# Performance work log

Hardware: AMD Instinct MI355X
Metric: run time of the kernel (lower is better)

Reference implementation:

```python
import jax, jax.numpy as jnp
import numpy as np

NEG_SLOPE = 0.2  # PyG GATConv default negative_slope
EPS = 1e-16     # PyG softmax denominator epsilon


def gat_conv(x, src, dst, W, a_src, a_dst, bias):
    """PyG GATConv (concat=True, dropout off). x:[N,Fin], src/dst:[E]."""
    N = x.shape[0]
    H, C = a_src.shape
    h = (x @ W).reshape(N, H, C)                      # per-head projected features
    es = jnp.einsum('nhc,hc->nh', h, a_src)           # alpha_src per node/head
    ed = jnp.einsum('nhc,hc->nh', h, a_dst)           # alpha_dst per node/head
    e = jax.nn.leaky_relu(es[src] + ed[dst], NEG_SLOPE)   # [E,H] edge scores
    # segment softmax over destination nodes (every node has a self loop)
    m = jax.ops.segment_max(e, dst, num_segments=N)
    p = jnp.exp(e - m[dst])
    denom = jax.ops.segment_sum(p, dst, num_segments=N)
    alpha = p / (denom[dst] + EPS)                    # [E,H]
    out = jax.ops.segment_sum(h[src] * alpha[:, :, None], dst, num_segments=N)
    return out.reshape(N, H * C) + bias


def _single_graph(x, ei, W1, a_src1, a_dst1, b1, W2, a_src2, a_dst2, b2):
    N = x.shape[0]
    loop = jnp.arange(N, dtype=ei.dtype)              # add_self_loops=True
    src = jnp.concatenate([ei[0], loop])
    dst = jnp.concatenate([ei[1], loop])
    h = jax.nn.relu(gat_conv(x, src, dst, W1, a_src1, a_dst1, b1))
    # F.dropout with p=0.0 is identity
    return gat_conv(h, src, dst, W2, a_src2, a_dst2, b2)


def setup_inputs() -> dict:
    key = jax.random.key(0)
    ks = jax.random.split(key, 9)
    B, N, E, F_in, H, C = 2, 20000, 320000, 128, 8, 64

    def glorot(k, shape):
        fan_in, fan_out = shape[-2] if len(shape) > 1 else shape[-1], shape[-1]
        s = np.sqrt(6.0 / (fan_in + fan_out)).astype(np.float32)
        return jax.random.uniform(k, shape, jnp.float32, -s, s)

    return {
        'xs': jax.random.normal(ks[0], (B, N, F_in), jnp.float32),
        'edge_indexs': jax.random.randint(ks[1], (B, 2, E), 0, N, jnp.int32),
        'W1': glorot(ks[2], (F_in, H * C)),
        'a_src1': glorot(ks[3], (H, C)),
        'a_dst1': glorot(ks[4], (H, C)),
        'b1': jnp.zeros((H * C,), jnp.float32),
        'W2': glorot(ks[5], (H * C, C)),
        'a_src2': glorot(ks[6], (1, C)),
        'a_dst2': glorot(ks[7], (1, C)),
        'b2': jnp.zeros((C,), jnp.float32),
    }


def reference(xs, edge_indexs, W1, a_src1, a_dst1, b1, W2, a_src2, a_dst2, b2):
    f = lambda x, ei: _single_graph(x, ei, W1, a_src1, a_dst1, b1, W2, a_src2, a_dst2, b2)
    return jax.vmap(f)(xs, edge_indexs)               # [B, N, C]
```

## Files before the change

kernel.cpp:

```cpp
#include <hip/hip_runtime.h>
#include <hip/hip_bf16.h>
#include <cstdint>

#define NEG_SLOPE 0.2f
#define SOFTMAX_EPS 1e-16f
#define NN 20000
#define EE 320000
#define CAP 48

typedef __hip_bfloat16 bf16;
typedef unsigned short ushort;
typedef short s8v __attribute__((ext_vector_type(8)));
typedef float f4v __attribute__((ext_vector_type(4)));
typedef float f2v __attribute__((ext_vector_type(2)));

static __device__ __forceinline__ float lo16(unsigned u) { return __uint_as_float(u << 16); }
static __device__ __forceinline__ float hi16(unsigned u) { return __uint_as_float(u & 0xffff0000u); }
static __device__ __forceinline__ ushort f2bf(float v) {
    bf16 h = __float2bfloat16(v);
    return *(ushort*)&h;
}

__global__ void prep_kernel(const float* __restrict__ W1, const float* __restrict__ W2,
                            ushort* __restrict__ w1hi, ushort* __restrict__ w1lo,
                            ushort* __restrict__ w2hi, ushort* __restrict__ w2lo,
                            int* __restrict__ count) {
    int bid = blockIdx.x;
    int t = threadIdx.x;
    if (bid >= 48) {
        int idx = (bid - 48) * 256 + t;
        if (idx < 2 * NN) count[idx] = 0;
        return;
    }
    __shared__ float T[32][65];
    const float* src; ushort *dhi, *dlo; int K, C, c0, k0;
    if (bid < 32) { src = W1; dhi = w1hi; dlo = w1lo; K = 128; C = 512; c0 = (bid & 7) * 64; k0 = (bid >> 3) * 32; }
    else          { src = W2; dhi = w2hi; dlo = w2lo; K = 512; C = 64;  c0 = 0;              k0 = (bid - 32) * 32; }
    for (int i = 0; i < 8; ++i) {
        int flat = t + i * 256;
        int k = flat >> 6, c = flat & 63;
        T[k][c] = src[(size_t)(k0 + k) * C + c0 + c];
    }
    __syncthreads();
    int c = t >> 2, j0 = (t & 3) * 8;
    unsigned hp[4], lp[4];
#pragma unroll
    for (int p = 0; p < 4; ++p) {
        float v0 = T[j0 + p * 2][c], v1 = T[j0 + p * 2 + 1][c];
        ushort h0 = f2bf(v0), h1 = f2bf(v1);
        float l0 = v0 - __uint_as_float((unsigned)h0 << 16);
        float l1 = v1 - __uint_as_float((unsigned)h1 << 16);
        hp[p] = (unsigned)h0 | ((unsigned)h1 << 16);
        lp[p] = (unsigned)f2bf(l0) | ((unsigned)f2bf(l1) << 16);
    }
    size_t o = (size_t)(c0 + c) * K + k0 + j0;
    *(uint4*)&dhi[o] = make_uint4(hp[0], hp[1], hp[2], hp[3]);
    *(uint4*)&dlo[o] = make_uint4(lp[0], lp[1], lp[2], lp[3]);
}

#define G1S 40
#define GEMM1_BLOCKS 1252
__global__ __launch_bounds__(256) void gemm1_scatter(
        const float* __restrict__ xs, const ushort* __restrict__ w1hi,
        const ushort* __restrict__ w1lo, const float* __restrict__ a_src,
        const float* __restrict__ a_dst, bf16* __restrict__ h1,
        float* __restrict__ es, float* __restrict__ ed,
        const int* __restrict__ ei, int* __restrict__ count,
        ushort* __restrict__ esrc) {
    __shared__ ushort lds[25600];
    int t = threadIdx.x;
    int bid = blockIdx.x;

    if (bid >= GEMM1_BLOCKS) {
        int idx = bid - GEMM1_BLOCKS;
        int b = idx / 1250;
        int e = (idx % 1250) * 256 + t;
        const int* srcA = ei + (size_t)b * 2 * EE;
        int s = srcA[e], d = srcA[EE + e];
        if ((unsigned)d >= NN || (unsigned)s >= NN) return;
        int pos = atomicAdd(&count[b * NN + d], 1);
        if (pos < CAP)
            esrc[((size_t)b * NN + d) * CAP + pos] = (ushort)s;
        return;
    }

    ushort* Xhi = lds;
    ushort* Xlo = lds + 2560;
    ushort* Whi = lds + 5120;
    ushort* Wlo = lds + 15360;
    int w = t >> 6, lane = t & 63, quad = lane >> 4, l16 = lane & 15;
    int b = bid / 626;
    int rem = bid % 626;
    int nhalf = rem / 313;
    int row0 = (rem % 313) * 64, nbase = nhalf * 256;
    const float* x = xs + (size_t)b * NN * 128;
    bf16*  h1b = h1 + (size_t)b * NN * 512;
    float* esb = es + (size_t)b * NN * 8;
    float* edb = ed + (size_t)b * NN * 8;

    f4v acc[16];
#pragma unroll
    for (int i = 0; i < 16; ++i) acc[i] = (f4v)0.f;

    for (int kc = 0; kc < 4; ++kc) {
        __syncthreads();
        {
            int row = t >> 2, c0 = (t & 3) * 8;
            float v[8];
            if (row0 + row < NN) {
                float4 A = *(const float4*)&x[(size_t)(row0 + row) * 128 + kc * 32 + c0];
                float4 B = *(const float4*)&x[(size_t)(row0 + row) * 128 + kc * 32 + c0 + 4];
                v[0] = A.x; v[1] = A.y; v[2] = A.z; v[3] = A.w;
                v[4] = B.x; v[5] = B.y; v[6] = B.z; v[7] = B.w;
            } else {
#pragma unroll
                for (int i = 0; i < 8; ++i) v[i] = 0.f;
            }
            unsigned hp[4], lp[4];
#pragma unroll
            for (int p = 0; p < 4; ++p) {
                ushort h0 = f2bf(v[p * 2]), h1_ = f2bf(v[p * 2 + 1]);
                float l0 = v[p * 2] - __uint_as_float((unsigned)h0 << 16);
                float l1 = v[p * 2 + 1] - __uint_as_float((unsigned)h1_ << 16);
                hp[p] = (unsigned)h0 | ((unsigned)h1_ << 16);
                lp[p] = (unsigned)f2bf(l0) | ((unsigned)f2bf(l1) << 16);
            }
            *(uint4*)&Xhi[row * G1S + c0] = make_uint4(hp[0], hp[1], hp[2], hp[3]);
            *(uint4*)&Xlo[row * G1S + c0] = make_uint4(lp[0], lp[1], lp[2], lp[3]);
        }
        {
            const ushort* sh = w1hi + (size_t)(nbase + t) * 128 + kc * 32;
            const ushort* sl = w1lo + (size_t)(nbase + t) * 128 + kc * 32;
            uint4 h0 = *(const uint4*)(sh), h1_ = *(const uint4*)(sh + 8);
            uint4 h2 = *(const uint4*)(sh + 16), h3 = *(const uint4*)(sh + 24);
            uint4 l0 = *(const uint4*)(sl), l1 = *(const uint4*)(sl + 8);
            uint4 l2 = *(const uint4*)(sl + 16), l3 = *(const uint4*)(sl + 24);
            *(uint4*)&Whi[t * G1S]      = h0; *(uint4*)&Whi[t * G1S + 8]  = h1_;
            *(uint4*)&Whi[t * G1S + 16] = h2; *(uint4*)&Whi[t * G1S + 24] = h3;
            *(uint4*)&Wlo[t * G1S]      = l0; *(uint4*)&Wlo[t * G1S + 8]  = l1;
            *(uint4*)&Wlo[t * G1S + 16] = l2; *(uint4*)&Wlo[t * G1S + 24] = l3;
        }
        __syncthreads();
        int arow = (w * 16 + l16) * G1S + quad * 8;
        s8v ahi = *(const s8v*)&Xhi[arow];
        s8v alo = *(const s8v*)&Xlo[arow];
#pragma unroll
        for (int ct = 0; ct < 16; ++ct) {
            int baddr = (ct * 16 + l16) * G1S + quad * 8;
            s8v bhi = *(const s8v*)&Whi[baddr];
            s8v blo = *(const s8v*)&Wlo[baddr];
            acc[ct] = __builtin_amdgcn_mfma_f32_16x16x32_bf16(ahi, bhi, acc[ct], 0, 0, 0);
            acc[ct] = __builtin_amdgcn_mfma_f32_16x16x32_bf16(ahi, blo, acc[ct], 0, 0, 0);
            acc[ct] = __builtin_amdgcn_mfma_f32_16x16x32_bf16(alo, bhi, acc[ct], 0, 0, 0);
        }
    }

#pragma unroll
    for (int hh = 0; hh < 4; ++hh) {
        float s4[4] = {0.f, 0.f, 0.f, 0.f}, d4[4] = {0.f, 0.f, 0.f, 0.f};
#pragma unroll
        for (int ct4 = 0; ct4 < 4; ++ct4) {
            int ct = hh * 4 + ct4;
            int c = nbase + ct * 16 + l16;
            float as = a_src[c], ad = a_dst[c];
#pragma unroll
            for (int r = 0; r < 4; ++r) { s4[r] += acc[ct][r] * as; d4[r] += acc[ct][r] * ad; }
        }
#pragma unroll
        for (int o = 1; o < 16; o <<= 1) {
#pragma unroll
            for (int r = 0; r < 4; ++r) {
                s4[r] += __shfl_xor(s4[r], o);
                d4[r] += __shfl_xor(d4[r], o);
            }
        }
        if (l16 == 0) {
            int head = nhalf * 4 + hh;
#pragma unroll
            for (int r = 0; r < 4; ++r) {
                int gr = row0 + w * 16 + quad * 4 + r;
                if (gr < NN) { esb[gr * 8 + head] = s4[r]; edb[gr * 8 + head] = d4[r]; }
            }
        }
    }

    __syncthreads();
    ushort* rp = lds + w * 4224;
#pragma unroll
    for (int ct = 0; ct < 16; ++ct)
#pragma unroll
        for (int r = 0; r < 4; ++r)
            rp[(quad * 4 + r) * 264 + ct * 16 + l16] = f2bf(acc[ct][r]);
#pragma unroll
    for (int i = 0; i < 8; ++i) {
        int idx = i * 512 + lane * 8;
        int row = idx >> 8, col = idx & 255;
        uint4 vv = *(const uint4*)&rp[row * 264 + col];
        int gr = row0 + w * 16 + row;
        if (gr < NN) *(uint4*)&h1b[(size_t)gr * 512 + nbase + col] = vv;
    }
}

#define G2S 72
__global__ __launch_bounds__(256) void gemm2_mfma(
        const bf16* __restrict__ a, const ushort* __restrict__ w2hi,
        const ushort* __restrict__ w2lo, const float* __restrict__ a_src,
        const float* __restrict__ a_dst, bf16* __restrict__ h2,
        float* __restrict__ es, float* __restrict__ ed) {
    __shared__ ushort lds[13824];
    ushort* AS  = lds;
    ushort* Whi = lds + 4608;
    ushort* Wlo = lds + 9216;

    int t = threadIdx.x;
    int w = t >> 6, lane = t & 63, quad = lane >> 4, l16 = lane & 15;
    int b = blockIdx.y;
    int row0 = blockIdx.x * 64;
    const bf16* ab = a + (size_t)b * NN * 512;
    bf16*  h2b = h2 + (size_t)b * NN * 64;
    float* esb = es + (size_t)b * NN;
    float* edb = ed + (size_t)b * NN;

    f4v acc[4];
#pragma unroll
    for (int i = 0; i < 4; ++i) acc[i] = (f4v)0.f;

    for (int kc = 0; kc < 8; ++kc) {
        __syncthreads();
        {
            int row = t >> 2, k0 = (t & 3) * 16;
            uint4 q0, q1;
            if (row0 + row < NN) {
                q0 = *(const uint4*)(ab + (size_t)(row0 + row) * 512 + kc * 64 + k0);
                q1 = *(const uint4*)(ab + (size_t)(row0 + row) * 512 + kc * 64 + k0 + 8);
            } else { q0 = make_uint4(0, 0, 0, 0); q1 = q0; }
            *(uint4*)&AS[row * G2S + k0]     = q0;
            *(uint4*)&AS[row * G2S + k0 + 8] = q1;
            const ushort* sh = w2hi + (size_t)row * 512 + kc * 64 + k0;
            const ushort* sl = w2lo + (size_t)row * 512 + kc * 64 + k0;
            *(uint4*)&Whi[row * G2S + k0]     = *(const uint4*)(sh);
            *(uint4*)&Whi[row * G2S + k0 + 8] = *(const uint4*)(sh + 8);
            *(uint4*)&Wlo[row * G2S + k0]     = *(const uint4*)(sl);
            *(uint4*)&Wlo[row * G2S + k0 + 8] = *(const uint4*)(sl + 8);
        }
        __syncthreads();
#pragma unroll
        for (int ks = 0; ks < 2; ++ks) {
            s8v av = *(const s8v*)&AS[(w * 16 + l16) * G2S + ks * 32 + quad * 8];
#pragma unroll
            for (int ct = 0; ct < 4; ++ct) {
                int baddr = (ct * 16 + l16) * G2S + ks * 32 + quad * 8;
                s8v bhi = *(const s8v*)&Whi[baddr];
                s8v blo = *(const s8v*)&Wlo[baddr];
                acc[ct] = __builtin_amdgcn_mfma_f32_16x16x32_bf16(av, bhi, acc[ct], 0, 0, 0);
                acc[ct] = __builtin_amdgcn_mfma_f32_16x16x32_bf16(av, blo, acc[ct], 0, 0, 0);
            }
        }
    }

    {
        float s4[4] = {0.f, 0.f, 0.f, 0.f}, d4[4] = {0.f, 0.f, 0.f, 0.f};
#pragma unroll
        for (int ct = 0; ct < 4; ++ct) {
            int c = ct * 16 + l16;
            float as = a_src[c], ad = a_dst[c];
#pragma unroll
            for (int r = 0; r < 4; ++r) { s4[r] += acc[ct][r] * as; d4[r] += acc[ct][r] * ad; }
        }
#pragma unroll
        for (int o = 1; o < 16; o <<= 1) {
#pragma unroll
            for (int r = 0; r < 4; ++r) {
                s4[r] += __shfl_xor(s4[r], o);
                d4[r] += __shfl_xor(d4[r], o);
            }
        }
        if (l16 == 0) {
#pragma unroll
            for (int r = 0; r < 4; ++r) {
                int gr = row0 + w * 16 + quad * 4 + r;
                if (gr < NN) { esb[gr] = s4[r]; edb[gr] = d4[r]; }
            }
        }
    }

    __syncthreads();
    ushort* rp = lds + w * 1152;
#pragma unroll
    for (int ct = 0; ct < 4; ++ct)
#pragma unroll
        for (int r = 0; r < 4; ++r)
            rp[(quad * 4 + r) * G2S + ct * 16 + l16] = f2bf(acc[ct][r]);
#pragma unroll
    for (int i = 0; i < 2; ++i) {
        int idx = i * 512 + lane * 8;
        int row = idx >> 6, col = idx & 63;
        uint4 vv = *(const uint4*)&rp[row * G2S + col];
        int gr = row0 + w * 16 + row;
        if (gr < NN) *(uint4*)&h2b[(size_t)gr * 64 + col] = vv;
    }
}

__global__ __launch_bounds__(256) void aggregate1_kernel(
        const bf16* __restrict__ h1, const float* __restrict__ es,
        const float* __restrict__ ed, const int* __restrict__ count,
        const ushort* __restrict__ esrc, const float* __restrict__ b1,
        bf16* __restrict__ out1) {
    __shared__ float alds[4][2][2][32];
    __shared__ unsigned offs[4][2][32];

    int t = threadIdx.x;
    int wv = t >> 6, lane = t & 63;
    int bid = blockIdx.x;
    int combo = bid & 7;
    int b = combo >> 2;
    int qtr = combo & 3;
    int nA = (bid >> 3) * 8 + wv * 2;
    int nd = lane >> 5;
    int slot = lane & 31;
    int n_lane = nA + nd;

    const bf16*  h1b = h1 + (size_t)b * NN * 512;
    const float* esb = es + (size_t)b * NN * 8;
    const float* edb = ed + (size_t)b * NN * 8;
    bf16* out1b = out1 + (size_t)b * NN * 512;

    int deg_e_lane = count[b * NN + n_lane];
    deg_e_lane = max(0, min(deg_e_lane, CAP));
    int degAe = __shfl(deg_e_lane, 0);
    int degBe = __shfl(deg_e_lane, 32);

    if (degAe > 31 || degBe > 31) {
        unsigned cb64 = (unsigned)qtr * 256u + (unsigned)lane * 4u;
        for (int k = 0; k < 2; ++k) {
            int nn = nA + k;
            int de = count[b * NN + nn];
            de = max(0, min(de, CAP));
            int dg = de + 1;
            bool act2 = lane < dg;
            int sr = act2 ? ((lane < de) ? (int)esrc[((size_t)b * NN + nn) * CAP + lane] : nn) : 0;
            float2 edv2 = *(const float2*)&edb[nn * 8 + qtr * 2];
            float2 esv2 = *(const float2*)((const char*)esb + ((unsigned)sr << 5) + (unsigned)qtr * 8u);
            float e0 = esv2.x + edv2.x; e0 = (e0 >= 0.f) ? e0 : NEG_SLOPE * e0; e0 = act2 ? e0 : -1e30f;
            float e1 = esv2.y + edv2.y; e1 = (e1 >= 0.f) ? e1 : NEG_SLOPE * e1; e1 = act2 ? e1 : -1e30f;
            float m0 = e0, m1 = e1;
#pragma unroll
            for (int o = 32; o > 0; o >>= 1) {
                m0 = fmaxf(m0, __shfl_xor(m0, o));
                m1 = fmaxf(m1, __shfl_xor(m1, o));
            }
            float p0 = act2 ? __expf(e0 - m0) : 0.f;
            float p1 = act2 ? __expf(e1 - m1) : 0.f;
            float s0 = p0, s1 = p1;
#pragma unroll
            for (int o = 32; o > 0; o >>= 1) {
                s0 += __shfl_xor(s0, o);
                s1 += __shfl_xor(s1, o);
            }
            float a0 = p0 / (s0 + SOFTMAX_EPS);
            float a1 = p1 / (s1 + SOFTMAX_EPS);
            f2v acc = {0.f, 0.f};
            for (int j = 0; j < dg; ++j) {
                int sj = __shfl(sr, j);
                float aw0 = __shfl(a0, j);
                float aw1 = __shfl(a1, j);
                float aw = (lane >= 32) ? aw1 : aw0;
                unsigned u = *(const unsigned*)((const char*)h1b + ((unsigned)sj << 10) + cb64);
                f2v tv = {lo16(u), hi16(u)};
                f2v wp2 = {aw, aw};
                acc += tv * wp2;
            }
            float2 bv2 = *(const float2*)&b1[qtr * 128 + lane * 2];
            union { ushort us[2]; unsigned u1; } pk;
            pk.us[0] = f2bf(fmaxf(acc.x + bv2.x, 0.f));
            pk.us[1] = f2bf(fmaxf(acc.y + bv2.y, 0.f));
            *(unsigned*)(out1b + (size_t)nn * 512 + qtr * 128 + lane * 2) = pk.u1;
        }
        return;
    }

    int deg = deg_e_lane + 1;
    bool act = slot < deg;
    size_t beg = ((size_t)b * NN + n_lane) * CAP;
    int sreg = act ? ((slot < deg_e_lane) ? (int)esrc[beg + slot] : n_lane) : 0;
    float2 edv = *(const float2*)&edb[n_lane * 8 + qtr * 2];
    float2 esv = *(const float2*)((const char*)esb + ((unsigned)sreg << 5) + (unsigned)qtr * 8u);
    float e0 = esv.x + edv.x; e0 = (e0 >= 0.f) ? e0 : NEG_SLOPE * e0; e0 = act ? e0 : -1e30f;
    float e1 = esv.y + edv.y; e1 = (e1 >= 0.f) ? e1 : NEG_SLOPE * e1; e1 = act ? e1 : -1e30f;
    float m0 = e0, m1 = e1;
#pragma unroll
    for (int o = 16; o > 0; o >>= 1) {
        m0 = fmaxf(m0, __shfl_xor(m0, o));
        m1 = fmaxf(m1, __shfl_xor(m1, o));
    }
    float p0 = act ? __expf(e0 - m0) : 0.f;
    float p1 = act ? __expf(e1 - m1) : 0.f;
    float s0 = p0, s1 = p1;
#pragma unroll
    for (int o = 16; o > 0; o >>= 1) {
        s0 += __shfl_xor(s0, o);
        s1 += __shfl_xor(s1, o);
    }
    offs[wv][nd][slot] = act ? ((unsigned)sreg << 10) : 0u;
    alds[wv][nd][0][slot] = p0 / (s0 + SOFTMAX_EPS);
    alds[wv][nd][1][slot] = p1 / (s1 + SOFTMAX_EPS);

    int mh = slot >> 4;
    const unsigned* op = &offs[wv][nd][0];
    const float*    wp = &alds[wv][nd][mh][0];
    unsigned cb = (unsigned)qtr * 256u + (unsigned)slot * 8u;
    const bf16* hb = h1b;
    int mdeg = max(degAe, degBe) + 1;
    int trips = (mdeg + 3) >> 2;
    int trips2 = (trips + 1) & ~1;

    f2v acc0 = {0.f, 0.f}, acc1 = {0.f, 0.f};
    uint2 A0, A1, A2, A3, B0, B1, B2, B3;
    float4 wA, wB;

#define GLOAD(dst, voff) \
    asm volatile("global_load_dwordx2 %0, %1, %2" : "=&v"(dst) : "v"(voff), "s"(hb))

#define LOADBANK(U0, U1, U2, U3, W4, blk) do { \
        int s_ = (blk) << 2; \
        uint4 ov_ = *(const uint4*)&op[s_]; \
        W4 = *(const float4*)&wp[s_]; \
        unsigned va_ = ov_.x + cb, vb_ = ov_.y + cb; \
        unsigned vc_ = ov_.z + cb, vd_ = ov_.w + cb; \
        GLOAD(U0, va_); GLOAD(U1, vb_); GLOAD(U2, vc_); GLOAD(U3, vd_); \
    } while (0)

#define WAITSB(nlit) do { \
        asm volatile("s_waitcnt vmcnt(" #nlit ")" ::: "memory"); \
        __builtin_amdgcn_sched_barrier(0); \
    } while (0)

#define ROW(U, W) do { \
        f2v wp_ = {W, W}; \
        f2v t0_ = {lo16(U.x), hi16(U.x)}; acc0 += t0_ * wp_; \
        f2v t1_ = {lo16(U.y), hi16(U.y)}; acc1 += t1_ * wp_; \
    } while (0)

#define CONSUME(U0, U1, U2, U3, W4) do { \
        ROW(U0, W4.x); ROW(U1, W4.y); ROW(U2, W4.z); ROW(U3, W4.w); \
    } while (0)

    LOADBANK(A0, A1, A2, A3, wA, 0);
    LOADBANK(B0, B1, B2, B3, wB, 1);
    for (int it = 0; it + 2 < trips2; it += 2) {
        WAITSB(4);
        CONSUME(A0, A1, A2, A3, wA); LOADBANK(A0, A1, A2, A3, wA, it + 2);
        WAITSB(4);
        CONSUME(B0, B1, B2, B3, wB); LOADBANK(B0, B1, B2, B3, wB, it + 3);
    }
    WAITSB(4);
    CONSUME(A0, A1, A2, A3, wA);
    WAITSB(0);
    CONSUME(B0, B1, B2, B3, wB);

#undef GLOAD
#undef LOADBANK
#undef WAITSB
#undef ROW
#undef CONSUME

    float4 bv = *(const float4*)&b1[qtr * 128 + slot * 4];
    union { ushort us[4]; uint2 u2; } pack;
    pack.us[0] = f2bf(fmaxf(acc0.x + bv.x, 0.f));
    pack.us[1] = f2bf(fmaxf(acc0.y + bv.y, 0.f));
    pack.us[2] = f2bf(fmaxf(acc1.x + bv.z, 0.f));
    pack.us[3] = f2bf(fmaxf(acc1.y + bv.w, 0.f));
    *(uint2*)(out1b + (size_t)n_lane * 512 + qtr * 128 + slot * 4) = pack.u2;
}

__global__ void aggregate2_kernel(const bf16* __restrict__ h2, const float* __restrict__ es,
                                  const float* __restrict__ ed, const int* __restrict__ count,
                                  const ushort* __restrict__ esrc, const float* __restrict__ bias2,
                                  float* __restrict__ out) {
    __shared__ float wl[4][64];
    __shared__ int slidx[4][64];
    int t = threadIdx.x;
    int wv = t >> 6, lane = t & 63;
    int bid = blockIdx.x;
    int xcd = bid & 7;
    int q = bid >> 3;
    int b = xcd >> 2;
    int n = (xcd & 3) * 5000 + q * 4 + wv;

    const bf16*  h2b = h2 + (size_t)b * NN * 64;
    const float* esb = es + (size_t)b * NN;
    const float* edb = ed + (size_t)b * NN;
    float* outb = out + (size_t)b * NN * 64;

    int deg_e = count[b * NN + n];
    deg_e = max(0, min(deg_e, CAP));
    int deg = deg_e + 1;
    size_t beg = ((size_t)b * NN + n) * CAP;
    float edn = edb[n];

    bool act = lane < deg;
    int sreg = act ? ((lane < deg_e) ? (int)esrc[beg + lane] : n) : 0;
    float ev = act ? esb[sreg] + edn : -1e30f;
    ev = (ev >= 0.f) ? ev : NEG_SLOPE * ev;
    if (!act) ev = -1e30f;
    float m = ev;
#pragma unroll
    for (int o = 32; o > 0; o >>= 1) m = fmaxf(m, __shfl_xor(m, o));
    float p = act ? __expf(ev - m) : 0.f;
    float sum = p;
#pragma unroll
    for (int o = 32; o > 0; o >>= 1) sum += __shfl_xor(sum, o);
    slidx[wv][lane] = sreg;
    wl[wv][lane] = p / (sum + SOFTMAX_EPS);

    float acc[4] = {0.f, 0.f, 0.f, 0.f};
    int grp = lane >> 4, ch4 = (lane & 15) * 4;
    int j = grp;
    for (; j + 4 < deg; j += 8) {
        int sA = slidx[wv][j];     float wA = wl[wv][j];
        int sB = slidx[wv][j + 4]; float wB = wl[wv][j + 4];
        uint2 uA = *(const uint2*)(h2b + (size_t)sA * 64 + ch4);
        uint2 uB = *(const uint2*)(h2b + (size_t)sB * 64 + ch4);
        acc[0] += wA * lo16(uA.x); acc[1] += wA * hi16(uA.x);
        acc[2] += wA * lo16(uA.y); acc[3] += wA * hi16(uA.y);
        acc[0] += wB * lo16(uB.x); acc[1] += wB * hi16(uB.x);
        acc[2] += wB * lo16(uB.y); acc[3] += wB * hi16(uB.y);
    }
    for (; j < deg; j += 4) {
        int s = slidx[wv][j];
        float wt = wl[wv][j];
        uint2 u = *(const uint2*)(h2b + (size_t)s * 64 + ch4);
        acc[0] += wt * lo16(u.x); acc[1] += wt * hi16(u.x);
        acc[2] += wt * lo16(u.y); acc[3] += wt * hi16(u.y);
    }
#pragma unroll
    for (int i = 0; i < 4; ++i) {
        acc[i] += __shfl_xor(acc[i], 16);
        acc[i] += __shfl_xor(acc[i], 32);
    }
    if (lane < 16) {
        float4 o4;
        o4.x = acc[0] + bias2[ch4 + 0];
        o4.y = acc[1] + bias2[ch4 + 1];
        o4.z = acc[2] + bias2[ch4 + 2];
        o4.w = acc[3] + bias2[ch4 + 3];
        *(float4*)&outb[(size_t)n * 64 + ch4] = o4;
    }
}

extern "C" void kernel_launch(void* const* d_in, const int* in_sizes, int n_in,
                              void* d_out, int out_size, void* d_ws, size_t ws_size,
                              hipStream_t stream) {
    const float* xs     = (const float*)d_in[0];
    const int*   ei     = (const int*)d_in[1];
    const float* W1     = (const float*)d_in[2];
    const float* a_src1 = (const float*)d_in[3];
    const float* a_dst1 = (const float*)d_in[4];
    const float* b1     = (const float*)d_in[5];
    const float* W2     = (const float*)d_in[6];
    const float* a_src2 = (const float*)d_in[7];
    const float* a_dst2 = (const float*)d_in[8];
    const float* b2     = (const float*)d_in[9];
    float* out = (float*)d_out;

    const int B = 2;

    uintptr_t p = (uintptr_t)d_ws;
    auto alloc = [&](size_t bytes) {
        void* r = (void*)p;
        p += (bytes + 255) & ~(size_t)255;
        return r;
    };
    bf16* h1   = (bf16*)alloc((size_t)B * NN * 512 * 2);
    bf16* out1 = (bf16*)alloc((size_t)B * NN * 512 * 2);
    char* unionA = (char*)alloc((size_t)B * NN * 64 * 2);
    float*  es1   = (float*)unionA;
    float*  ed1   = (float*)(unionA + 1280000);
    ushort* wt1hi = (ushort*)(unionA + 2560000);
    ushort* wt1lo = (ushort*)(unionA + 2560000 + 131072);
    bf16*   h2    = (bf16*)unionA;
    ushort* wt2hi = (ushort*)alloc((size_t)64 * 512 * 2);
    ushort* wt2lo = (ushort*)alloc((size_t)64 * 512 * 2);
    float* es2    = (float*)alloc((size_t)B * NN * 4);
    float* ed2    = (float*)alloc((size_t)B * NN * 4);
    int*   count  = (int*)alloc((size_t)B * NN * 4);
    ushort* esrc  = (ushort*)alloc((size_t)B * NN * CAP * 2);

    const int initBlocks = (2 * NN + 255) / 256;
    prep_kernel<<<48 + initBlocks, 256, 0, stream>>>(W1, W2, wt1hi, wt1lo, wt2hi, wt2lo, count);
    gemm1_scatter<<<GEMM1_BLOCKS + 2500, 256, 0, stream>>>(xs, wt1hi, wt1lo, a_src1, a_dst1,
                                                           h1, es1, ed1, ei, count, esrc);
    aggregate1_kernel<<<20000, 256, 0, stream>>>(h1, es1, ed1, count, esrc, b1, out1);
    gemm2_mfma<<<dim3(313, B), 256, 0, stream>>>(out1, wt2hi, wt2lo, a_src2, a_dst2, h2, es2, ed2);
    aggregate2_kernel<<<10000, 256, 0, stream>>>(h2, es2, ed2, count, esrc, b2, out);
}
```

Baseline: 258.2 us.

## Precompute x bf16 hi/lo split in prep kernel and split aggregate1 per batch

Moves the fp32-to-bf16 hi/lo split of the input features out of the GEMM1 tile loader into the prep kernel, writing the split to a workspace reused from out1. GEMM1 then loads the pre-split bf16 data directly, saving conversion ALU work per tile and each tile's repeated conversion. Aggregate1 is launched once per batch, its block index remapped, and the h1 base pointer is made scalar with readfirstlane. h2 now aliases h1 with a 512-column stride. The cost is an extra pass over x in prep and an extra kernel launch.

```diff
diff --git a/kernel.cpp b/kernel.cpp
--- a/kernel.cpp
+++ b/kernel.cpp
@@ -22,11 +22,31 @@
 }
 
 __global__ void prep_kernel(const float* __restrict__ W1, const float* __restrict__ W2,
+                            const float* __restrict__ xs,
                             ushort* __restrict__ w1hi, ushort* __restrict__ w1lo,
                             ushort* __restrict__ w2hi, ushort* __restrict__ w2lo,
+                            ushort* __restrict__ xhi, ushort* __restrict__ xlo,
                             int* __restrict__ count) {
     int bid = blockIdx.x;
     int t = threadIdx.x;
+    if (bid >= 205) {
+        size_t idx = (size_t)(bid - 205) * 2048 + (size_t)t * 8;
+        float4 A = *(const float4*)&xs[idx];
+        float4 B = *(const float4*)&xs[idx + 4];
+        float v[8] = {A.x, A.y, A.z, A.w, B.x, B.y, B.z, B.w};
+        unsigned hp[4], lp[4];
+#pragma unroll
+        for (int p = 0; p < 4; ++p) {
+            ushort h0 = f2bf(v[p * 2]), h1 = f2bf(v[p * 2 + 1]);
+            float l0 = v[p * 2] - __uint_as_float((unsigned)h0 << 16);
+            float l1 = v[p * 2 + 1] - __uint_as_float((unsigned)h1 << 16);
+            hp[p] = (unsigned)h0 | ((unsigned)h1 << 16);
+            lp[p] = (unsigned)f2bf(l0) | ((unsigned)f2bf(l1) << 16);
+        }
+        *(uint4*)&xhi[idx] = make_uint4(hp[0], hp[1], hp[2], hp[3]);
+        *(uint4*)&xlo[idx] = make_uint4(lp[0], lp[1], lp[2], lp[3]);
+        return;
+    }
     if (bid >= 48) {
         int idx = (bid - 48) * 256 + t;
         if (idx < 2 * NN) count[idx] = 0;
@@ -59,41 +79,22 @@
 }
 
 #define G1S 40
-#define GEMM1_BLOCKS 1252
-__global__ __launch_bounds__(256) void gemm1_scatter(
-        const float* __restrict__ xs, const ushort* __restrict__ w1hi,
-        const ushort* __restrict__ w1lo, const float* __restrict__ a_src,
-        const float* __restrict__ a_dst, bf16* __restrict__ h1,
-        float* __restrict__ es, float* __restrict__ ed,
-        const int* __restrict__ ei, int* __restrict__ count,
-        ushort* __restrict__ esrc) {
+static __device__ void gemm1_body(int b, int rem,
+        const ushort* __restrict__ xhi, const ushort* __restrict__ xlo,
+        const ushort* __restrict__ w1hi, const ushort* __restrict__ w1lo,
+        const float* __restrict__ a_src, const float* __restrict__ a_dst,
+        bf16* __restrict__ h1, float* __restrict__ es, float* __restrict__ ed) {
     __shared__ ushort lds[25600];
     int t = threadIdx.x;
-    int bid = blockIdx.x;
-
-    if (bid >= GEMM1_BLOCKS) {
-        int idx = bid - GEMM1_BLOCKS;
-        int b = idx / 1250;
-        int e = (idx % 1250) * 256 + t;
-        const int* srcA = ei + (size_t)b * 2 * EE;
-        int s = srcA[e], d = srcA[EE + e];
-        if ((unsigned)d >= NN || (unsigned)s >= NN) return;
-        int pos = atomicAdd(&count[b * NN + d], 1);
-        if (pos < CAP)
-            esrc[((size_t)b * NN + d) * CAP + pos] = (ushort)s;
-        return;
-    }
-
     ushort* Xhi = lds;
     ushort* Xlo = lds + 2560;
     ushort* Whi = lds + 5120;
     ushort* Wlo = lds + 15360;
     int w = t >> 6, lane = t & 63, quad = lane >> 4, l16 = lane & 15;
-    int b = bid / 626;
-    int rem = bid % 626;
     int nhalf = rem / 313;
     int row0 = (rem % 313) * 64, nbase = nhalf * 256;
-    const float* x = xs + (size_t)b * NN * 128;
+    const ushort* xh = xhi + (size_t)b * NN * 128;
+    const ushort* xl = xlo + (size_t)b * NN * 128;
     bf16*  h1b = h1 + (size_t)b * NN * 512;
     float* esb = es + (size_t)b * NN * 8;
     float* edb = ed + (size_t)b * NN * 8;
@@ -106,27 +107,14 @@
         __syncthreads();
         {
             int row = t >> 2, c0 = (t & 3) * 8;
-            float v[8];
+            uint4 hv, lv;
             if (row0 + row < NN) {
-                float4 A = *(const float4*)&x[(size_t)(row0 + row) * 128 + kc * 32 + c0];
-                float4 B = *(const float4*)&x[(size_t)(row0 + row) * 128 + kc * 32 + c0 + 4];
-                v[0] = A.x; v[1] = A.y; v[2] = A.z; v[3] = A.w;
-                v[4] = B.x; v[5] = B.y; v[6] = B.z; v[7] = B.w;
-            } else {
-#pragma unroll
-                for (int i = 0; i < 8; ++i) v[i] = 0.f;
-            }
-            unsigned hp[4], lp[4];
-#pragma unroll
-            for (int p = 0; p < 4; ++p) {
-                ushort h0 = f2bf(v[p * 2]), h1_ = f2bf(v[p * 2 + 1]);
-                float l0 = v[p * 2] - __uint_as_float((unsigned)h0 << 16);
-                float l1 = v[p * 2 + 1] - __uint_as_float((unsigned)h1_ << 16);
-                hp[p] = (unsigned)h0 | ((unsigned)h1_ << 16);
-                lp[p] = (unsigned)f2bf(l0) | ((unsigned)f2bf(l1) << 16);
-            }
-            *(uint4*)&Xhi[row * G1S + c0] = make_uint4(hp[0], hp[1], hp[2], hp[3]);
-            *(uint4*)&Xlo[row * G1S + c0] = make_uint4(lp[0], lp[1], lp[2], lp[3]);
+                size_t off = (size_t)(row0 + row) * 128 + kc * 32 + c0;
+                hv = *(const uint4*)&xh[off];
+                lv = *(const uint4*)&xl[off];
+            } else { hv = make_uint4(0, 0, 0, 0); lv = hv; }
+            *(uint4*)&Xhi[row * G1S + c0] = hv;
+            *(uint4*)&Xlo[row * G1S + c0] = lv;
         }
         {
             const ushort* sh = w1hi + (size_t)(nbase + t) * 128 + kc * 32;
@@ -201,23 +189,47 @@
     }
 }
 
+static __device__ void scatter_body(int idx, const int* __restrict__ ei,
+                                    int* __restrict__ count, ushort* __restrict__ esrc) {
+    int t = threadIdx.x;
+    int b = idx / 1250;
+    int e = (idx % 1250) * 256 + t;
+    const int* srcA = ei + (size_t)b * 2 * EE;
+    int s = srcA[e], d = srcA[EE + e];
+    if ((unsigned)d >= NN || (unsigned)s >= NN) return;
+    int pos = atomicAdd(&count[b * NN + d], 1);
+    if (pos < CAP)
+        esrc[((size_t)b * NN + d) * CAP + pos] = (ushort)s;
+}
+
+__global__ __launch_bounds__(256) void gemm1_scatter(
+        const ushort* __restrict__ xhi, const ushort* __restrict__ xlo,
+        const ushort* __restrict__ w1hi, const ushort* __restrict__ w1lo,
+        const float* __restrict__ a_src, const float* __restrict__ a_dst,
+        bf16* __restrict__ h1, float* __restrict__ es, float* __restrict__ ed,
+        const int* __restrict__ ei, int* __restrict__ count, ushort* __restrict__ esrc) {
+    int bid = blockIdx.x;
+    if (bid < 1252) gemm1_body(bid / 626, bid % 626, xhi, xlo, w1hi, w1lo, a_src, a_dst, h1, es, ed);
+    else            scatter_body(bid - 1252, ei, count, esrc);
+}
+
 #define G2S 72
 __global__ __launch_bounds__(256) void gemm2_mfma(
         const bf16* __restrict__ a, const ushort* __restrict__ w2hi,
         const ushort* __restrict__ w2lo, const float* __restrict__ a_src,
         const float* __restrict__ a_dst, bf16* __restrict__ h2,
         float* __restrict__ es, float* __restrict__ ed) {
-    __shared__ ushort lds[13824];
-    ushort* AS  = lds;
-    ushort* Whi = lds + 4608;
-    ushort* Wlo = lds + 9216;
+    __shared__ ushort lds2[13824];
+    ushort* AS  = lds2;
+    ushort* Whi = lds2 + 4608;
+    ushort* Wlo = lds2 + 9216;
 
     int t = threadIdx.x;
     int w = t >> 6, lane = t & 63, quad = lane >> 4, l16 = lane & 15;
     int b = blockIdx.y;
     int row0 = blockIdx.x * 64;
     const bf16* ab = a + (size_t)b * NN * 512;
-    bf16*  h2b = h2 + (size_t)b * NN * 64;
+    bf16*  h2b = h2 + (size_t)b * NN * 512;
     float* esb = es + (size_t)b * NN;
     float* edb = ed + (size_t)b * NN;
 
@@ -285,7 +297,7 @@
     }
 
     __syncthreads();
-    ushort* rp = lds + w * 1152;
+    ushort* rp = lds2 + w * 1152;
 #pragma unroll
     for (int ct = 0; ct < 4; ++ct)
 #pragma unroll
@@ -301,7 +313,7 @@
     }
 }
 
-__global__ __launch_bounds__(256) void aggregate1_kernel(
+__global__ __launch_bounds__(256) void aggregate1_kernel(int b,
         const bf16* __restrict__ h1, const float* __restrict__ es,
         const float* __restrict__ ed, const int* __restrict__ count,
         const ushort* __restrict__ esrc, const float* __restrict__ b1,
@@ -311,11 +323,10 @@
 
     int t = threadIdx.x;
     int wv = t >> 6, lane = t & 63;
-    int bid = blockIdx.x;
-    int combo = bid & 7;
-    int b = combo >> 2;
-    int qtr = combo & 3;
-    int nA = (bid >> 3) * 8 + wv * 2;
+    int j = blockIdx.x;
+    int qtr = (j & 7) >> 1;
+    int qidx = (j >> 3) * 2 + (j & 1);
+    int nA = qidx * 8 + wv * 2;
     int nd = lane >> 5;
     int slot = lane & 31;
     int n_lane = nA + nd;
@@ -360,10 +371,10 @@
             float a0 = p0 / (s0 + SOFTMAX_EPS);
             float a1 = p1 / (s1 + SOFTMAX_EPS);
             f2v acc = {0.f, 0.f};
-            for (int j = 0; j < dg; ++j) {
-                int sj = __shfl(sr, j);
-                float aw0 = __shfl(a0, j);
-                float aw1 = __shfl(a1, j);
+            for (int jj = 0; jj < dg; ++jj) {
+                int sj = __shfl(sr, jj);
+                float aw0 = __shfl(a0, jj);
+                float aw1 = __shfl(a1, jj);
                 float aw = (lane >= 32) ? aw1 : aw0;
                 unsigned u = *(const unsigned*)((const char*)h1b + ((unsigned)sj << 10) + cb64);
                 f2v tv = {lo16(u), hi16(u)};
@@ -409,7 +420,10 @@
     const unsigned* op = &offs[wv][nd][0];
     const float*    wp = &alds[wv][nd][mh][0];
     unsigned cb = (unsigned)qtr * 256u + (unsigned)slot * 8u;
-    const bf16* hb = h1b;
+    uint64_t hbu = (uint64_t)(uintptr_t)h1b;
+    unsigned hb_lo = __builtin_amdgcn_readfirstlane((unsigned)hbu);
+    unsigned hb_hi = __builtin_amdgcn_readfirstlane((unsigned)(hbu >> 32));
+    uint64_t hbs = ((uint64_t)hb_hi << 32) | (uint64_t)hb_lo;
     int mdeg = max(degAe, degBe) + 1;
     int trips = (mdeg + 3) >> 2;
     int trips2 = (trips + 1) & ~1;
@@ -419,7 +433,7 @@
     float4 wA, wB;
 
 #define GLOAD(dst, voff) \
-    asm volatile("global_load_dwordx2 %0, %1, %2" : "=&v"(dst) : "v"(voff), "s"(hb))
+    asm volatile("global_load_dwordx2 %0, %1, %2" : "=&v"(dst) : "v"(voff), "s"(hbs))
 
 #define LOADBANK(U0, U1, U2, U3, W4, blk) do { \
         int s_ = (blk) << 2; \
@@ -487,7 +501,7 @@
     int b = xcd >> 2;
     int n = (xcd & 3) * 5000 + q * 4 + wv;
 
-    const bf16*  h2b = h2 + (size_t)b * NN * 64;
+    const bf16*  h2b = h2 + (size_t)b * NN * 512;
     const float* esb = es + (size_t)b * NN;
     const float* edb = ed + (size_t)b * NN;
     float* outb = out + (size_t)b * NN * 64;
@@ -578,7 +592,9 @@
     float*  ed1   = (float*)(unionA + 1280000);
     ushort* wt1hi = (ushort*)(unionA + 2560000);
     ushort* wt1lo = (ushort*)(unionA + 2560000 + 131072);
-    bf16*   h2    = (bf16*)unionA;
+    bf16*   h2    = h1;
+    ushort* xhi   = (ushort*)out1;
+    ushort* xlo   = xhi + (size_t)B * NN * 128;
     ushort* wt2hi = (ushort*)alloc((size_t)64 * 512 * 2);
     ushort* wt2lo = (ushort*)alloc((size_t)64 * 512 * 2);
     float* es2    = (float*)alloc((size_t)B * NN * 4);
@@ -586,11 +602,12 @@
     int*   count  = (int*)alloc((size_t)B * NN * 4);
     ushort* esrc  = (ushort*)alloc((size_t)B * NN * CAP * 2);
 
-    const int initBlocks = (2 * NN + 255) / 256;
-    prep_kernel<<<48 + initBlocks, 256, 0, stream>>>(W1, W2, wt1hi, wt1lo, wt2hi, wt2lo, count);
-    gemm1_scatter<<<GEMM1_BLOCKS + 2500, 256, 0, stream>>>(xs, wt1hi, wt1lo, a_src1, a_dst1,
-                                                           h1, es1, ed1, ei, count, esrc);
-    aggregate1_kernel<<<20000, 256, 0, stream>>>(h1, es1, ed1, count, esrc, b1, out1);
+    prep_kernel<<<2705, 256, 0, stream>>>(W1, W2, xs, wt1hi, wt1lo, wt2hi, wt2lo,
+                                          xhi, xlo, count);
+    gemm1_scatter<<<1252 + 2500, 256, 0, stream>>>(xhi, xlo, wt1hi, wt1lo, a_src1, a_dst1,
+                                                   h1, es1, ed1, ei, count, esrc);
+    aggregate1_kernel<<<10000, 256, 0, stream>>>(0, h1, es1, ed1, count, esrc, b1, out1);
+    aggregate1_kernel<<<10000, 256, 0, stream>>>(1, h1, es1, ed1, count, esrc, b1, out1);
     gemm2_mfma<<<dim3(313, B), 256, 0, stream>>>(out1, wt2hi, wt2lo, a_src2, a_dst2, h2, es2, ed2);
     aggregate2_kernel<<<10000, 256, 0, stream>>>(h2, es2, ed2, count, esrc, b2, out);
 }
```

Result: slower. 279.5 us (+8.2%).
